# Performance work log

Measured on AMD Instinct MI355X. Metric: run time of the kernel, lower is better.

The kernel has to match this reference:

```python
import jax, jax.numpy as jnp
import numpy as np

N = 50000        # num nodes
NFEAT = 512      # input feature dim
NCLASS = 256     # output classes (out_features of out_att)
E_RAND = 800000  # random edges; + N self-loops
NEG_SLOPE = 0.2  # leakyrelu alpha


def setup_inputs() -> dict:
    key = jax.random.key(0)
    k1, k2, k3, k4 = jax.random.split(key, 4)
    x = jax.random.normal(k1, (N, NFEAT), dtype=jnp.float32)
    W = jax.random.normal(k2, (NFEAT, NCLASS), dtype=jnp.float32) / np.float32(np.sqrt(NFEAT))
    a = jax.random.normal(k3, (2 * NCLASS,), dtype=jnp.float32) / np.float32(np.sqrt(2 * NCLASS))
    rand_edges = jax.random.randint(k4, (2, E_RAND), 0, N, dtype=jnp.int32)
    self_loops = jnp.tile(jnp.arange(N, dtype=jnp.int32), (2, 1))
    edge_index = jnp.concatenate([rand_edges, self_loops], axis=1)  # [2, E]
    return {"x": x, "W": W, "a": a, "edge_index": edge_index}


def reference(x, W, a, edge_index):
    # Eval-mode SpGAT: dropout is identity (training=False).
    row, col = edge_index[0], edge_index[1]  # edge = adj.nonzero().t(): row aggregates from col
    h = x @ W                                # [N, F]
    F_out = h.shape[1]
    # a @ cat(h[row], h[col]) == (h @ a1)[row] + (h @ a2)[col]  (avoids [E, 2F] concat)
    s_row = h @ a[:F_out]                    # [N]
    s_col = h @ a[F_out:]                    # [N]
    logits = s_row[row] + s_col[col]         # [E]
    e = jnp.exp(-jax.nn.leaky_relu(logits, negative_slope=NEG_SLOPE))  # [E]
    rowsum = jax.ops.segment_sum(e, row, num_segments=N)               # [N]
    msgs = e[:, None] * h[col]                                         # [E, F]
    h_prime = jax.ops.segment_sum(msgs, row, num_segments=N) / rowsum[:, None]
    return jax.nn.log_softmax(jax.nn.elu(h_prime), axis=1)
```

## Files before the change

kernel.cpp:

```cpp
#include <hip/hip_runtime.h>
#include <math.h>

#define NNODES   50000
#define NFEAT    512
#define NCLASS   256
#define NEG_SLOPE 0.2f
#define GBLK     782
#define BCAP     64

typedef __attribute__((ext_vector_type(8))) short short8;
typedef __attribute__((ext_vector_type(4))) float floatx4;

__device__ __forceinline__ unsigned short f2bf(float f) {
    unsigned u = __builtin_bit_cast(unsigned, f);
    u += 0x7fffu + ((u >> 16) & 1u);
    return (unsigned short)(u >> 16);
}
__device__ __forceinline__ float bf2f_lo(unsigned u) {
    return __builtin_bit_cast(float, u << 16);
}
__device__ __forceinline__ float bf2f_hi(unsigned u) {
    return __builtin_bit_cast(float, u & 0xffff0000u);
}
__device__ __forceinline__ unsigned pack_bf16_rh(float lo, float hi) {
    const unsigned ulo = __builtin_bit_cast(unsigned, lo) + 0x8000u;
    const unsigned uhi = __builtin_bit_cast(unsigned, hi) + 0x8000u;
    return __builtin_amdgcn_perm(uhi, ulo, 0x07060302);
}

#if __has_builtin(__builtin_amdgcn_fdot2_f32_bf16)
#define HAVE_DOT2 1
typedef __attribute__((ext_vector_type(2))) __bf16 bfx2;
__device__ __forceinline__ float dot2bf(unsigned hpair, unsigned epair, float acc) {
    return __builtin_amdgcn_fdot2_f32_bf16(__builtin_bit_cast(bfx2, hpair),
                                           __builtin_bit_cast(bfx2, epair), acc, false);
}
#endif

__global__ __launch_bounds__(256) void init_kernel(const float* __restrict__ W,
                                                   unsigned short* __restrict__ Wt,
                                                   int* __restrict__ cursor, int zn) {
    const int i = blockIdx.x * 256 + threadIdx.x;
    const int n = i >> 9;
    const int k = i & 511;
    Wt[i] = f2bf(W[(size_t)k * NCLASS + n]);
    if (i < zn) cursor[i] = 0;
}

__global__ __launch_bounds__(256, 4) void gemm_mfma_kernel(const float* __restrict__ x,
                                                           const unsigned short* __restrict__ Wt,
                                                           unsigned short* __restrict__ hb,
                                                           const float* __restrict__ a,
                                                           float* __restrict__ s_row,
                                                           float* __restrict__ s_col,
                                                           const int* __restrict__ erow,
                                                           const int* __restrict__ ecol,
                                                           int* __restrict__ cursor,
                                                           int* __restrict__ bucket,
                                                           int M, int E) {
    __shared__ union {
        struct { short As[2][64 * 32]; short Bs[2][256 * 32]; } k;
        short Cs[32 * 260];
    } u;

    const int tid  = threadIdx.x;
    const int w    = tid >> 6;
    const int lane = tid & 63;
    const int rowbase = blockIdx.x * 64;

    const int wm = w & 1;
    const int wn = w >> 1;
    const int srow = lane >> 2;
    const int skq  = (lane & 3) << 3;
    const int fm = lane & 15;
    const int fq = lane >> 4;

    floatx4 acc[2][8];
#pragma unroll
    for (int i = 0; i < 2; ++i)
#pragma unroll
        for (int j = 0; j < 8; ++j)
            acc[i][j] = (floatx4){0.f, 0.f, 0.f, 0.f};

    const int arow = min(rowbase + w * 16 + srow, M - 1);
    const size_t abase = (size_t)arow * NFEAT + skq;
    const int lrowA = (w * 16 + srow) * 32 + skq;

#define STAGE_B(buf, k0)                                                                      \
    {                                                                                         \
        _Pragma("unroll")                                                                     \
        for (int t = 0; t < 4; ++t) {                                                         \
            const int seg = w * 4 + t;                                                        \
            const int nr  = seg * 16 + srow;                                                  \
            __builtin_amdgcn_global_load_lds(                                                 \
                (const __attribute__((address_space(1))) void*)(Wt + (size_t)nr * NFEAT + (k0) + skq), \
                (__attribute__((address_space(3))) void*)(&u.k.Bs[buf][seg * 512]), 16, 0, 0); \
        }                                                                                     \
    }

    STAGE_B(0, 0)
    {
        const float4* xp = (const float4*)&x[abase];
        const float4 u0 = xp[0];
        const float4 u1 = xp[1];
        uint4 o;
        o.x = pack_bf16_rh(u0.x, u0.y);
        o.y = pack_bf16_rh(u0.z, u0.w);
        o.z = pack_bf16_rh(u1.x, u1.y);
        o.w = pack_bf16_rh(u1.z, u1.w);
        *(uint4*)&u.k.As[0][lrowA] = o;
    }
    __syncthreads();

    int cur = 0;
    for (int k0 = 0; k0 < NFEAT; k0 += 32) {
        const int nxt = cur ^ 1;
        const bool have_next = (k0 + 32) < NFEAT;
        float4 p0, p1;
        if (have_next) {
            const float4* xp = (const float4*)&x[abase + k0 + 32];
            p0 = xp[0];
            p1 = xp[1];
            STAGE_B(nxt, k0 + 32)
        }

        short8 af[2];
#pragma unroll
        for (int mt = 0; mt < 2; ++mt)
            af[mt] = *(const short8*)&u.k.As[cur][(wm * 32 + mt * 16 + fm) * 32 + fq * 8];
#pragma unroll
        for (int nt = 0; nt < 8; ++nt) {
            const short8 bfr = *(const short8*)&u.k.Bs[cur][(wn * 128 + nt * 16 + fm) * 32 + fq * 8];
            acc[0][nt] = __builtin_amdgcn_mfma_f32_16x16x32_bf16(af[0], bfr, acc[0][nt], 0, 0, 0);
            acc[1][nt] = __builtin_amdgcn_mfma_f32_16x16x32_bf16(af[1], bfr, acc[1][nt], 0, 0, 0);
        }

        if (have_next) {
            uint4 o;
            o.x = pack_bf16_rh(p0.x, p0.y);
            o.y = pack_bf16_rh(p0.z, p0.w);
            o.z = pack_bf16_rh(p1.x, p1.y);
            o.w = pack_bf16_rh(p1.z, p1.w);
            *(uint4*)&u.k.As[nxt][lrowA] = o;
        }
        __syncthreads();
        cur = nxt;
    }

#pragma unroll
    for (int p = 0; p < 2; ++p) {
        __syncthreads();
        if (wm == p) {
#pragma unroll
            for (int mt = 0; mt < 2; ++mt)
#pragma unroll
                for (int nt = 0; nt < 8; ++nt)
#pragma unroll
                    for (int r = 0; r < 4; ++r)
                        u.Cs[(mt * 16 + fq * 4 + r) * 260 + wn * 128 + nt * 16 + fm] =
                            (short)f2bf(acc[mt][nt][r]);
        }
        __syncthreads();
#pragma unroll
        for (int kk = 0; kk < 8; ++kk) {
            const int idx = tid + kk * 256;
            const int lrow = idx >> 6;
            const int c4 = (idx & 63) << 2;
            const int grow = rowbase + p * 32 + lrow;
            const uint2 vv = *(const uint2*)&u.Cs[lrow * 260 + c4];
            const float f0 = bf2f_lo(vv.x), f1 = bf2f_hi(vv.x);
            const float f2 = bf2f_lo(vv.y), f3 = bf2f_hi(vv.y);
            const float4 A1 = *(const float4*)&a[c4];
            const float4 A2 = *(const float4*)&a[NCLASS + c4];
            float p1 = f0 * A1.x + f1 * A1.y + f2 * A1.z + f3 * A1.w;
            float p2 = f0 * A2.x + f1 * A2.y + f2 * A2.z + f3 * A2.w;
#pragma unroll
            for (int off = 1; off < 64; off <<= 1) {
                p1 += __shfl_xor(p1, off);
                p2 += __shfl_xor(p2, off);
            }
            if (grow < M) {
                *(uint2*)&hb[(size_t)grow * NCLASS + c4] = vv;
                if (lane == 0) {
                    s_row[grow] = p1;
                    s_col[grow] = p2;
                }
            }
        }
    }

    const int gtid = blockIdx.x * 256 + tid;
    for (int i = gtid; i < E; i += GBLK * 256) {
        const int r = erow[i];
        const int c = ecol[i];
        const int pos = atomicAdd(&cursor[r], 1);
        if (pos < BCAP) bucket[((size_t)r << 6) + pos] = c;
    }
}

__global__ __launch_bounds__(256) void aggregate_kernel(const unsigned short* __restrict__ hb,
                                                        const int* __restrict__ bucket,
                                                        const int* __restrict__ cnt,
                                                        const float* __restrict__ s_row,
                                                        const float* __restrict__ s_col,
                                                        float* __restrict__ out, int n) {
    const int wave = (int)((blockIdx.x * (size_t)blockDim.x + threadIdx.x) >> 6);
    const int lane = threadIdx.x & 63;
    if (wave >= n) return;
    const int r = wave;
    const int jb = r << 6;
    const int je = jb + min(cnt[r], BCAP);
    const int fo = lane << 2;
    const float sr = s_row[r];

    float rowsum = 0.f;
    int j = jb;

#define EDGE_E(c) ({ const float _l = sr + s_col[c];                         \
                     const float _lr = _l > 0.f ? _l : NEG_SLOPE * _l;       \
                     __expf(-_lr); })

#ifdef HAVE_DOT2
    float ac0 = 0.f, ac1 = 0.f, ac2 = 0.f, ac3 = 0.f;
    for (; j + 3 < je; j += 4) {
        const int4 cv = *(const int4*)&bucket[j];
        const uint2 g0 = *(const uint2*)&hb[(size_t)cv.x * NCLASS + fo];
        const uint2 g1 = *(const uint2*)&hb[(size_t)cv.y * NCLASS + fo];
        const uint2 g2 = *(const uint2*)&hb[(size_t)cv.z * NCLASS + fo];
        const uint2 g3 = *(const uint2*)&hb[(size_t)cv.w * NCLASS + fo];
        const float e0 = EDGE_E(cv.x);
        const float e1 = EDGE_E(cv.y);
        const float e2 = EDGE_E(cv.z);
        const float e3 = EDGE_E(cv.w);
        const unsigned ep01 = pack_bf16_rh(e0, e1);
        const unsigned ep23 = pack_bf16_rh(e2, e3);
        rowsum += (e0 + e1) + (e2 + e3);
        ac0 = dot2bf(__builtin_amdgcn_perm(g1.x, g0.x, 0x05040100), ep01, ac0);
        ac1 = dot2bf(__builtin_amdgcn_perm(g1.x, g0.x, 0x07060302), ep01, ac1);
        ac2 = dot2bf(__builtin_amdgcn_perm(g1.y, g0.y, 0x05040100), ep01, ac2);
        ac3 = dot2bf(__builtin_amdgcn_perm(g1.y, g0.y, 0x07060302), ep01, ac3);
        ac0 = dot2bf(__builtin_amdgcn_perm(g3.x, g2.x, 0x05040100), ep23, ac0);
        ac1 = dot2bf(__builtin_amdgcn_perm(g3.x, g2.x, 0x07060302), ep23, ac1);
        ac2 = dot2bf(__builtin_amdgcn_perm(g3.y, g2.y, 0x05040100), ep23, ac2);
        ac3 = dot2bf(__builtin_amdgcn_perm(g3.y, g2.y, 0x07060302), ep23, ac3);
    }
    float4 acc = make_float4(ac0, ac1, ac2, ac3);
#else
    float4 acc = make_float4(0.f, 0.f, 0.f, 0.f);
    for (; j + 3 < je; j += 4) {
        const int4 cv = *(const int4*)&bucket[j];
        const uint2 g0 = *(const uint2*)&hb[(size_t)cv.x * NCLASS + fo];
        const uint2 g1 = *(const uint2*)&hb[(size_t)cv.y * NCLASS + fo];
        const uint2 g2 = *(const uint2*)&hb[(size_t)cv.z * NCLASS + fo];
        const uint2 g3 = *(const uint2*)&hb[(size_t)cv.w * NCLASS + fo];
        const float e0 = EDGE_E(cv.x);
        const float e1 = EDGE_E(cv.y);
        const float e2 = EDGE_E(cv.z);
        const float e3 = EDGE_E(cv.w);
        rowsum += (e0 + e1) + (e2 + e3);
        acc.x += e0 * bf2f_lo(g0.x) + e1 * bf2f_lo(g1.x) + e2 * bf2f_lo(g2.x) + e3 * bf2f_lo(g3.x);
        acc.y += e0 * bf2f_hi(g0.x) + e1 * bf2f_hi(g1.x) + e2 * bf2f_hi(g2.x) + e3 * bf2f_hi(g3.x);
        acc.z += e0 * bf2f_lo(g0.y) + e1 * bf2f_lo(g1.y) + e2 * bf2f_lo(g2.y) + e3 * bf2f_lo(g3.y);
        acc.w += e0 * bf2f_hi(g0.y) + e1 * bf2f_hi(g1.y) + e2 * bf2f_hi(g2.y) + e3 * bf2f_hi(g3.y);
    }
#endif
    for (; j < je; ++j) {
        const int c = bucket[j];
        const uint2 g = *(const uint2*)&hb[(size_t)c * NCLASS + fo];
        const float e = EDGE_E(c);
        rowsum += e;
        acc.x += e * bf2f_lo(g.x);
        acc.y += e * bf2f_hi(g.x);
        acc.z += e * bf2f_lo(g.y);
        acc.w += e * bf2f_hi(g.y);
    }

    const float inv = 1.f / rowsum;
    float v[4] = {acc.x * inv, acc.y * inv, acc.z * inv, acc.w * inv};
#pragma unroll
    for (int i = 0; i < 4; ++i)
        v[i] = v[i] > 0.f ? v[i] : __expf(v[i]) - 1.f;

    float m = fmaxf(fmaxf(v[0], v[1]), fmaxf(v[2], v[3]));
#pragma unroll
    for (int off = 32; off > 0; off >>= 1) m = fmaxf(m, __shfl_xor(m, off));
    float s = 0.f;
#pragma unroll
    for (int i = 0; i < 4; ++i) s += __expf(v[i] - m);
#pragma unroll
    for (int off = 32; off > 0; off >>= 1) s += __shfl_xor(s, off);
    const float lse = m + __logf(s);

    float4 o = make_float4(v[0] - lse, v[1] - lse, v[2] - lse, v[3] - lse);
    *(float4*)&out[(size_t)r * NCLASS + fo] = o;
}

extern "C" void kernel_launch(void* const* d_in, const int* in_sizes, int n_in,
                              void* d_out, int out_size, void* d_ws, size_t ws_size,
                              hipStream_t stream) {
    const float* x  = (const float*)d_in[0];
    const float* W  = (const float*)d_in[1];
    const float* a  = (const float*)d_in[2];
    const int* edge = (const int*)d_in[3];
    float* out = (float*)d_out;

    const int M = in_sizes[0] / NFEAT;
    const int E = in_sizes[3] / 2;
    const int* row = edge;
    const int* col = edge + E;

    char* ws = (char*)d_ws;
    size_t off = 0;
    auto carve = [&](size_t bytes) -> char* {
        char* p = ws + off;
        off = (off + bytes + 255) & ~(size_t)255;
        return p;
    };
    unsigned short* Wt = (unsigned short*)carve((size_t)NCLASS * NFEAT * sizeof(short));
    unsigned short* hb = (unsigned short*)carve((size_t)M * NCLASS * sizeof(short));
    int*   cursor   = (int*)carve((size_t)M * sizeof(int));
    float* s_row    = (float*)carve((size_t)M * sizeof(float));
    float* s_col    = (float*)carve((size_t)M * sizeof(float));
    int*   bucket   = (int*)carve((size_t)M * BCAP * sizeof(int));

    init_kernel<<<512, 256, 0, stream>>>(W, Wt, cursor, M);

    gemm_mfma_kernel<<<GBLK, 256, 0, stream>>>(x, Wt, hb, a, s_row, s_col,
                                               row, col, cursor, bucket, M, E);

    aggregate_kernel<<<(M + 3) / 4, 256, 0, stream>>>(hb, bucket, cursor, s_row, s_col, out, M);
}
```

Baseline: 314.9 us.

## Halve GEMM row tile to 32 and split edge bucketing into separate kernel

```diff
diff --git a/kernel.cpp b/kernel.cpp
--- a/kernel.cpp
+++ b/kernel.cpp
@@ -5,7 +5,7 @@
 #define NFEAT    512
 #define NCLASS   256
 #define NEG_SLOPE 0.2f
-#define GBLK     782
+#define GBLK     1564
 #define BCAP     64
 
 typedef __attribute__((ext_vector_type(8))) short short8;
@@ -53,62 +53,54 @@
                                                            const float* __restrict__ a,
                                                            float* __restrict__ s_row,
                                                            float* __restrict__ s_col,
-                                                           const int* __restrict__ erow,
-                                                           const int* __restrict__ ecol,
-                                                           int* __restrict__ cursor,
-                                                           int* __restrict__ bucket,
-                                                           int M, int E) {
+                                                           int M) {
     __shared__ union {
-        struct { short As[2][64 * 32]; short Bs[2][256 * 32]; } k;
+        struct { short As[2][32 * 32]; short Bs[2][256 * 32]; } k;
         short Cs[32 * 260];
     } u;
 
     const int tid  = threadIdx.x;
     const int w    = tid >> 6;
     const int lane = tid & 63;
-    const int rowbase = blockIdx.x * 64;
-
-    const int wm = w & 1;
-    const int wn = w >> 1;
-    const int srow = lane >> 2;
-    const int skq  = (lane & 3) << 3;
+    const int rowbase = blockIdx.x * 32;
+
     const int fm = lane & 15;
     const int fq = lane >> 4;
 
-    floatx4 acc[2][8];
+    floatx4 acc[2][4];
 #pragma unroll
     for (int i = 0; i < 2; ++i)
 #pragma unroll
-        for (int j = 0; j < 8; ++j)
+        for (int j = 0; j < 4; ++j)
             acc[i][j] = (floatx4){0.f, 0.f, 0.f, 0.f};
 
-    const int arow = min(rowbase + w * 16 + srow, M - 1);
-    const size_t abase = (size_t)arow * NFEAT + skq;
-    const int lrowA = (w * 16 + srow) * 32 + skq;
-
+    const int srowA = lane >> 3;
+    const int skqA  = (lane & 7) << 2;
+    const int arow  = min(rowbase + w * 8 + srowA, M - 1);
+    const size_t abase = (size_t)arow * NFEAT + skqA;
+    const int lrowA = (w * 8 + srowA) * 32 + skqA;
+
+    const int srowB = lane >> 2;
+    const int skqB  = (lane & 3) << 3;
 #define STAGE_B(buf, k0)                                                                      \
     {                                                                                         \
         _Pragma("unroll")                                                                     \
         for (int t = 0; t < 4; ++t) {                                                         \
             const int seg = w * 4 + t;                                                        \
-            const int nr  = seg * 16 + srow;                                                  \
+            const int nr  = seg * 16 + srowB;                                                 \
             __builtin_amdgcn_global_load_lds(                                                 \
-                (const __attribute__((address_space(1))) void*)(Wt + (size_t)nr * NFEAT + (k0) + skq), \
+                (const __attribute__((address_space(1))) void*)(Wt + (size_t)nr * NFEAT + (k0) + skqB), \
                 (__attribute__((address_space(3))) void*)(&u.k.Bs[buf][seg * 512]), 16, 0, 0); \
         }                                                                                     \
     }
 
     STAGE_B(0, 0)
     {
-        const float4* xp = (const float4*)&x[abase];
-        const float4 u0 = xp[0];
-        const float4 u1 = xp[1];
-        uint4 o;
+        const float4 u0 = *(const float4*)&x[abase];
+        uint2 o;
         o.x = pack_bf16_rh(u0.x, u0.y);
         o.y = pack_bf16_rh(u0.z, u0.w);
-        o.z = pack_bf16_rh(u1.x, u1.y);
-        o.w = pack_bf16_rh(u1.z, u1.w);
-        *(uint4*)&u.k.As[0][lrowA] = o;
+        *(uint2*)&u.k.As[0][lrowA] = o;
     }
     __syncthreads();
 
@@ -116,86 +108,81 @@
     for (int k0 = 0; k0 < NFEAT; k0 += 32) {
         const int nxt = cur ^ 1;
         const bool have_next = (k0 + 32) < NFEAT;
-        float4 p0, p1;
+        float4 p0;
         if (have_next) {
-            const float4* xp = (const float4*)&x[abase + k0 + 32];
-            p0 = xp[0];
-            p1 = xp[1];
+            p0 = *(const float4*)&x[abase + k0 + 32];
             STAGE_B(nxt, k0 + 32)
         }
 
         short8 af[2];
 #pragma unroll
         for (int mt = 0; mt < 2; ++mt)
-            af[mt] = *(const short8*)&u.k.As[cur][(wm * 32 + mt * 16 + fm) * 32 + fq * 8];
-#pragma unroll
-        for (int nt = 0; nt < 8; ++nt) {
-            const short8 bfr = *(const short8*)&u.k.Bs[cur][(wn * 128 + nt * 16 + fm) * 32 + fq * 8];
+            af[mt] = *(const short8*)&u.k.As[cur][(mt * 16 + fm) * 32 + fq * 8];
+#pragma unroll
+        for (int nt = 0; nt < 4; ++nt) {
+            const short8 bfr = *(const short8*)&u.k.Bs[cur][(w * 64 + nt * 16 + fm) * 32 + fq * 8];
             acc[0][nt] = __builtin_amdgcn_mfma_f32_16x16x32_bf16(af[0], bfr, acc[0][nt], 0, 0, 0);
             acc[1][nt] = __builtin_amdgcn_mfma_f32_16x16x32_bf16(af[1], bfr, acc[1][nt], 0, 0, 0);
         }
 
         if (have_next) {
-            uint4 o;
+            uint2 o;
             o.x = pack_bf16_rh(p0.x, p0.y);
             o.y = pack_bf16_rh(p0.z, p0.w);
-            o.z = pack_bf16_rh(p1.x, p1.y);
-            o.w = pack_bf16_rh(p1.z, p1.w);
-            *(uint4*)&u.k.As[nxt][lrowA] = o;
+            *(uint2*)&u.k.As[nxt][lrowA] = o;
         }
         __syncthreads();
         cur = nxt;
     }
 
-#pragma unroll
-    for (int p = 0; p < 2; ++p) {
-        __syncthreads();
-        if (wm == p) {
-#pragma unroll
-            for (int mt = 0; mt < 2; ++mt)
-#pragma unroll
-                for (int nt = 0; nt < 8; ++nt)
-#pragma unroll
-                    for (int r = 0; r < 4; ++r)
-                        u.Cs[(mt * 16 + fq * 4 + r) * 260 + wn * 128 + nt * 16 + fm] =
-                            (short)f2bf(acc[mt][nt][r]);
-        }
-        __syncthreads();
-#pragma unroll
-        for (int kk = 0; kk < 8; ++kk) {
-            const int idx = tid + kk * 256;
-            const int lrow = idx >> 6;
-            const int c4 = (idx & 63) << 2;
-            const int grow = rowbase + p * 32 + lrow;
-            const uint2 vv = *(const uint2*)&u.Cs[lrow * 260 + c4];
-            const float f0 = bf2f_lo(vv.x), f1 = bf2f_hi(vv.x);
-            const float f2 = bf2f_lo(vv.y), f3 = bf2f_hi(vv.y);
-            const float4 A1 = *(const float4*)&a[c4];
-            const float4 A2 = *(const float4*)&a[NCLASS + c4];
-            float p1 = f0 * A1.x + f1 * A1.y + f2 * A1.z + f3 * A1.w;
-            float p2 = f0 * A2.x + f1 * A2.y + f2 * A2.z + f3 * A2.w;
-#pragma unroll
-            for (int off = 1; off < 64; off <<= 1) {
-                p1 += __shfl_xor(p1, off);
-                p2 += __shfl_xor(p2, off);
+    __syncthreads();
+#pragma unroll
+    for (int mt = 0; mt < 2; ++mt)
+#pragma unroll
+        for (int nt = 0; nt < 4; ++nt)
+#pragma unroll
+            for (int r = 0; r < 4; ++r)
+                u.Cs[(mt * 16 + fq * 4 + r) * 260 + w * 64 + nt * 16 + fm] =
+                    (short)f2bf(acc[mt][nt][r]);
+    __syncthreads();
+#pragma unroll
+    for (int kk = 0; kk < 8; ++kk) {
+        const int idx = tid + kk * 256;
+        const int lrow = idx >> 6;
+        const int c4 = (idx & 63) << 2;
+        const int grow = rowbase + lrow;
+        const uint2 vv = *(const uint2*)&u.Cs[lrow * 260 + c4];
+        const float f0 = bf2f_lo(vv.x), f1 = bf2f_hi(vv.x);
+        const float f2 = bf2f_lo(vv.y), f3 = bf2f_hi(vv.y);
+        const float4 A1 = *(const float4*)&a[c4];
+        const float4 A2 = *(const float4*)&a[NCLASS + c4];
+        float p1 = f0 * A1.x + f1 * A1.y + f2 * A1.z + f3 * A1.w;
+        float p2 = f0 * A2.x + f1 * A2.y + f2 * A2.z + f3 * A2.w;
+#pragma unroll
+        for (int off = 1; off < 64; off <<= 1) {
+            p1 += __shfl_xor(p1, off);
+            p2 += __shfl_xor(p2, off);
+        }
+        if (grow < M) {
+            *(uint2*)&hb[(size_t)grow * NCLASS + c4] = vv;
+            if (lane == 0) {
+                s_row[grow] = p1;
+                s_col[grow] = p2;
             }
-            if (grow < M) {
-                *(uint2*)&hb[(size_t)grow * NCLASS + c4] = vv;
-                if (lane == 0) {
-                    s_row[grow] = p1;
-                    s_col[grow] = p2;
-                }
-            }
-        }
-    }
-
-    const int gtid = blockIdx.x * 256 + tid;
-    for (int i = gtid; i < E; i += GBLK * 256) {
-        const int r = erow[i];
-        const int c = ecol[i];
-        const int pos = atomicAdd(&cursor[r], 1);
-        if (pos < BCAP) bucket[((size_t)r << 6) + pos] = c;
-    }
+        }
+    }
+}
+
+__global__ __launch_bounds__(256) void scatter_kernel(const int* __restrict__ row,
+                                                      const int* __restrict__ col,
+                                                      int* __restrict__ cursor,
+                                                      int* __restrict__ bucket, int e) {
+    const int i = blockIdx.x * 256 + threadIdx.x;
+    if (i >= e) return;
+    const int r = row[i];
+    const int c = col[i];
+    const int pos = atomicAdd(&cursor[r], 1);
+    if (pos < BCAP) bucket[((size_t)r << 6) + pos] = c;
 }
 
 __global__ __launch_bounds__(256) void aggregate_kernel(const unsigned short* __restrict__ hb,
@@ -325,8 +312,9 @@
 
     init_kernel<<<512, 256, 0, stream>>>(W, Wt, cursor, M);
 
-    gemm_mfma_kernel<<<GBLK, 256, 0, stream>>>(x, Wt, hb, a, s_row, s_col,
-                                               row, col, cursor, bucket, M, E);
+    gemm_mfma_kernel<<<GBLK, 256, 0, stream>>>(x, Wt, hb, a, s_row, s_col, M);
+
+    scatter_kernel<<<(E + 255) / 256, 256, 0, stream>>>(row, col, cursor, bucket, E);
 
     aggregate_kernel<<<(M + 3) / 4, 256, 0, stream>>>(hb, bucket, cursor, s_row, s_col, out, M);
 }
```

Result: no change. 314.1 us (-0.2%).
